# Kernel tuning notes

Measured on AMD Instinct MI355X. Metric: run time of the kernel, lower is better.

## Reference

```python
import jax, jax.numpy as jnp
import numpy as np

B, NX, NY, CIN = 4, 128, 128, 64
D, H = 64, 8  # out_channels, nhead
EPS = 1e-5


def setup_inputs() -> dict:
    key = jax.random.key(0)
    ks = jax.random.split(key, 12)
    s_in = 1.0 / np.sqrt(CIN)
    s_hd = 1.0 / np.sqrt(H * D)
    return {
        "v": jax.random.normal(ks[0], (B, NX, NY, CIN), jnp.float32),
        "Wq_w": jax.random.uniform(ks[1], (CIN, H * D), jnp.float32, -s_in, s_in),
        "Wq_b": jax.random.uniform(ks[2], (H * D,), jnp.float32, -s_in, s_in),
        "Wk_w": jax.random.uniform(ks[3], (CIN, H * D), jnp.float32, -s_in, s_in),
        "Wk_b": jax.random.uniform(ks[4], (H * D,), jnp.float32, -s_in, s_in),
        "Wv_w": jax.random.uniform(ks[5], (CIN, H * D), jnp.float32, -s_in, s_in),
        "Wv_b": jax.random.uniform(ks[6], (H * D,), jnp.float32, -s_in, s_in),
        "lnq_g": jnp.ones((H, D), jnp.float32),
        "lnq_b": jnp.zeros((H, D), jnp.float32),
        "lnk_g": jnp.ones((H, D), jnp.float32),
        "lnk_b": jnp.zeros((H, D), jnp.float32),
        "Wo_w": jax.random.uniform(ks[7], (H * D, D), jnp.float32, -s_hd, s_hd),
        "Wo_b": jax.random.uniform(ks[8], (D,), jnp.float32, -s_hd, s_hd),
    }


def _layernorm(x, gamma, beta):
    # x: [b,h,n,d]; gamma/beta: [h,d] (per-head params)
    mu = jnp.mean(x, axis=-1, keepdims=True)
    var = jnp.mean(jnp.square(x - mu), axis=-1, keepdims=True)
    xn = (x - mu) * jax.lax.rsqrt(var + EPS)
    return xn * gamma[None, :, None, :] + beta[None, :, None, :]


def reference(v, Wq_w, Wq_b, Wk_w, Wk_b, Wv_w, Wv_b,
              lnq_g, lnq_b, lnk_g, lnk_b, Wo_w, Wo_b):
    b, nx, ny, _ = v.shape
    n = nx * ny
    vf = v.reshape(b, n, -1)  # [b, n, cin]
    # QKV projections -> [b, h, n, d]
    def proj(w, bias):
        y = vf @ w + bias  # [b, n, h*d]
        return y.reshape(b, n, H, D).transpose(0, 2, 1, 3)
    Q = _layernorm(proj(Wq_w, Wq_b), lnq_g, lnq_b)
    K = _layernorm(proj(Wk_w, Wk_b), lnk_g, lnk_b)
    V = proj(Wv_w, Wv_b)
    # Non-softmax linear attention: (Q K^T) V == Q (K^T V); use O(n d^2) form
    kv = jnp.einsum('bhnd,bhne->bhde', K, V)      # [b,h,d,d]
    attn = jnp.einsum('bhmd,bhde->bhme', Q, kv)   # [b,h,n,d]
    attn = attn.transpose(0, 2, 1, 3).reshape(b, n, H * D)
    out = (attn @ Wo_w + Wo_b) / n
    return out.reshape(b, nx, ny, D)
```

## Files before the change

### kernel.cpp

```cpp
#include <hip/hip_runtime.h>

typedef __attribute__((ext_vector_type(8))) short bhalf8;
typedef __attribute__((ext_vector_type(4))) float f32x4;

#define MFMA_BF16 __builtin_amdgcn_mfma_f32_16x16x32_bf16

namespace {

constexpr int   NPIX  = 16384;
constexpr float EPSV  = 1e-5f;
constexpr float INV64 = 1.0f / 64.0f;
constexpr float INV_N = 1.0f / 16384.0f;

__device__ __forceinline__ unsigned short f2bf(float f) {
    unsigned int u = __builtin_bit_cast(unsigned int, f);
    u += 0x7fffu + ((u >> 16) & 1u);
    return (unsigned short)(u >> 16);
}

__global__ void k0_vsum(const float* __restrict__ v, float* __restrict__ vsum)
{
    const int slab = blockIdx.x, b = blockIdx.y, t = threadIdx.x;
    const int c = t & 63, po = t >> 6;
    const float* src = v + ((size_t)b * NPIX + slab * 256 + po * 64) * 64 + c;
    float s = 0.f;
#pragma unroll 8
    for (int i = 0; i < 64; ++i) s += src[(size_t)i * 64];
    __shared__ float red[4][64];
    red[po][c] = s;
    __syncthreads();
    if (t < 64) {
        float x = red[0][t] + red[1][t] + red[2][t] + red[3][t];
        atomicAdd(vsum + b * 64 + t, x);
    }
}

__global__ __launch_bounds__(256, 2)
void k1_kv(const float* __restrict__ v,  const float* __restrict__ Wk,
           const float* __restrict__ bk, const float* __restrict__ Wv,
           const float* __restrict__ bv, float* __restrict__ kvG)
{
    const int ch = blockIdx.x, h = blockIdx.y, b = blockIdx.z;
    const int t = threadIdx.x;
    const int w = t >> 6, l = t & 63, g = l >> 4, m16 = l & 15;

    __shared__ float kvred[4][4096];
    char* zone = reinterpret_cast<char*>(&kvred[0][0]) + w * 14848;
    unsigned short* vz  = reinterpret_cast<unsigned short*>(zone);
    unsigned short* ktz = reinterpret_cast<unsigned short*>(zone + 4608);
    unsigned short* vtz = reinterpret_cast<unsigned short*>(zone + 9728);

    bhalf8 wkf[4][2], wvf[4][2];
    const int wcol = h * 64 + m16;
#pragma unroll
    for (int mt = 0; mt < 4; ++mt)
#pragma unroll
      for (int ks = 0; ks < 2; ++ks)
#pragma unroll
        for (int j = 0; j < 8; ++j) {
            const int c = 32 * ks + 8 * g + j;
            wkf[mt][ks][j] = (short)f2bf(Wk[c * 512 + wcol + 16 * mt]);
            wvf[mt][ks][j] = (short)f2bf(Wv[c * 512 + wcol + 16 * mt]);
        }
    float bkr[4][4], bvr[4][4];
#pragma unroll
    for (int mt = 0; mt < 4; ++mt)
#pragma unroll
      for (int q = 0; q < 4; ++q) {
          const int d = 16 * mt + 4 * g + q;
          bkr[mt][q] = bk[h * 64 + d];
          bvr[mt][q] = bv[h * 64 + d];
      }

    f32x4 kv[4][4];
#pragma unroll
    for (int i = 0; i < 4; ++i)
#pragma unroll
      for (int j2 = 0; j2 < 4; ++j2) kv[i][j2] = f32x4{0.f, 0.f, 0.f, 0.f};

    const float* vbase = v + ((size_t)b * NPIX + ch * 1024 + w * 256) * 64;
    const int sp = l >> 1, sh = l & 1;

    for (int s = 0; s < 8; ++s) {
        {
            const float4* src = reinterpret_cast<const float4*>(
                vbase + (size_t)(s * 32 + sp) * 64 + sh * 32);
            unsigned short* dst = vz + sp * 72 + sh * 32;
#pragma unroll
            for (int qq = 0; qq < 8; ++qq) {
                float4 x = src[qq];
                ushort4 o;
                o.x = f2bf(x.x); o.y = f2bf(x.y); o.z = f2bf(x.z); o.w = f2bf(x.w);
                *reinterpret_cast<ushort4*>(dst + qq * 4) = o;
            }
        }
        __builtin_amdgcn_sched_barrier(0);
        bhalf8 vf[2][2];
#pragma unroll
        for (int nt = 0; nt < 2; ++nt)
#pragma unroll
          for (int ks = 0; ks < 2; ++ks)
            vf[nt][ks] = *reinterpret_cast<const bhalf8*>(
                vz + (16 * nt + m16) * 72 + 32 * ks + 8 * g);

#pragma unroll
        for (int mt = 0; mt < 4; ++mt)
#pragma unroll
          for (int nt = 0; nt < 2; ++nt) {
              f32x4 a = {0.f, 0.f, 0.f, 0.f};
              a = MFMA_BF16(wvf[mt][0], vf[nt][0], a, 0, 0, 0);
              a = MFMA_BF16(wvf[mt][1], vf[nt][1], a, 0, 0, 0);
#pragma unroll
              for (int q = 0; q < 4; ++q)
                  vtz[(16 * mt + 4 * g + q) * 40 + 16 * nt + m16] =
                      f2bf(a[q] + bvr[mt][q]);
          }

        f32x4 pa[4][2];
#pragma unroll
        for (int mt = 0; mt < 4; ++mt)
#pragma unroll
          for (int nt = 0; nt < 2; ++nt) {
              f32x4 a = {0.f, 0.f, 0.f, 0.f};
              a = MFMA_BF16(wkf[mt][0], vf[nt][0], a, 0, 0, 0);
              a = MFMA_BF16(wkf[mt][1], vf[nt][1], a, 0, 0, 0);
#pragma unroll
              for (int q = 0; q < 4; ++q) a[q] += bkr[mt][q];
              pa[mt][nt] = a;
          }
#pragma unroll
        for (int nt = 0; nt < 2; ++nt) {
            float s1 = 0.f, s2 = 0.f;
#pragma unroll
            for (int mt = 0; mt < 4; ++mt)
#pragma unroll
              for (int q = 0; q < 4; ++q) {
                  float x = pa[mt][nt][q]; s1 += x; s2 = fmaf(x, x, s2);
              }
            s1 += __shfl_xor(s1, 16, 64); s1 += __shfl_xor(s1, 32, 64);
            s2 += __shfl_xor(s2, 16, 64); s2 += __shfl_xor(s2, 32, 64);
            const float mu = s1 * INV64;
            const float rs = rsqrtf(fmaxf(s2 * INV64 - mu * mu, 0.f) + EPSV);
#pragma unroll
            for (int mt = 0; mt < 4; ++mt)
#pragma unroll
              for (int q = 0; q < 4; ++q)
                  ktz[(16 * mt + 4 * g + q) * 40 + 16 * nt + m16] =
                      f2bf((pa[mt][nt][q] - mu) * rs);
        }
        __builtin_amdgcn_sched_barrier(0);

        bhalf8 ka[4], vb2[4];
#pragma unroll
        for (int mt = 0; mt < 4; ++mt)
            ka[mt] = *reinterpret_cast<const bhalf8*>(ktz + (16 * mt + m16) * 40 + 8 * g);
#pragma unroll
        for (int nt = 0; nt < 4; ++nt)
            vb2[nt] = *reinterpret_cast<const bhalf8*>(vtz + (16 * nt + m16) * 40 + 8 * g);
#pragma unroll
        for (int mt = 0; mt < 4; ++mt)
#pragma unroll
          for (int nt = 0; nt < 4; ++nt)
              kv[mt][nt] = MFMA_BF16(ka[mt], vb2[nt], kv[mt][nt], 0, 0, 0);
        __builtin_amdgcn_sched_barrier(0);
    }

    __syncthreads();
#pragma unroll
    for (int mt = 0; mt < 4; ++mt)
#pragma unroll
      for (int nt = 0; nt < 4; ++nt)
#pragma unroll
        for (int q = 0; q < 4; ++q)
            kvred[w][(16 * mt + 4 * g + q) * 64 + 16 * nt + m16] = kv[mt][nt][q];
    __syncthreads();
    float* dstg = kvG + ((size_t)(b * 8 + h)) * 4096;
#pragma unroll
    for (int i = 0; i < 16; ++i) {
        const int idx = i * 256 + t;
        const float srd = kvred[0][idx] + kvred[1][idx] + kvred[2][idx] + kvred[3][idx];
        atomicAdd(dstg + idx, srd);
    }
}

__global__ void k2_mix(const float* __restrict__ kvG,  const float* __restrict__ vsum,
                       const float* __restrict__ Wv,   const float* __restrict__ bv,
                       const float* __restrict__ lnkg, const float* __restrict__ lnkb,
                       const float* __restrict__ lnqg, const float* __restrict__ lnqb,
                       const float* __restrict__ Wo,   const float* __restrict__ Wob,
                       unsigned short* __restrict__ MTp, float* __restrict__ cbeta)
{
    const int h = blockIdx.x, b = blockIdx.y, t = threadIdx.x;
    __shared__ float kvs[64][65], wos[64][65], mts[64][65], Svs[64], us[64];
    const int r = t >> 2, c0 = (t & 3) * 16;
    const float* kg = kvG + ((size_t)(b * 8 + h)) * 4096;
#pragma unroll
    for (int i = 0; i < 16; i += 4) {
        float4 x = *reinterpret_cast<const float4*>(kg + r * 64 + c0 + i);
        kvs[r][c0+i] = x.x; kvs[r][c0+i+1] = x.y; kvs[r][c0+i+2] = x.z; kvs[r][c0+i+3] = x.w;
    }
#pragma unroll
    for (int i = 0; i < 16; i += 4) {
        float4 x = *reinterpret_cast<const float4*>(Wo + ((size_t)(h * 64) + r) * 64 + c0 + i);
        wos[r][c0+i] = x.x; wos[r][c0+i+1] = x.y; wos[r][c0+i+2] = x.z; wos[r][c0+i+3] = x.w;
    }
    if (t < 64) {
        float s = 16384.f * bv[h * 64 + t];
        for (int cc = 0; cc < 64; ++cc)
            s = fmaf(vsum[b * 64 + cc], Wv[cc * 512 + h * 64 + t], s);
        Svs[t] = s;
    }
    __syncthreads();
    {
        const float gk = lnkg[h * 64 + r], bk2 = lnkb[h * 64 + r];
#pragma unroll
        for (int i = 0; i < 16; ++i)
            kvs[r][c0 + i] = gk * kvs[r][c0 + i] + bk2 * Svs[c0 + i];
    }
    __syncthreads();
    if (t < 64) {
        float s = 0.f;
        for (int dd = 0; dd < 64; ++dd) s = fmaf(lnqb[h * 64 + dd], kvs[dd][t], s);
        us[t] = s;
    }
    float mrow[16];
#pragma unroll
    for (int i = 0; i < 16; ++i) mrow[i] = 0.f;
    for (int e2 = 0; e2 < 64; ++e2) {
        const float kr = kvs[r][e2];
#pragma unroll
        for (int i = 0; i < 16; ++i) mrow[i] = fmaf(kr, wos[e2][c0 + i], mrow[i]);
    }
    {
        const float gq = lnqg[h * 64 + r] * INV_N;
#pragma unroll
        for (int i = 0; i < 16; ++i) mts[c0 + i][r] = gq * mrow[i];
    }
    __syncthreads();
    if (t < 64) {
        float s = 0.f;
        for (int e2 = 0; e2 < 64; ++e2) s = fmaf(us[e2], wos[e2][t], s);
        atomicAdd(cbeta + b * 64 + t, s * INV_N);
        if (h == 0) atomicAdd(cbeta + b * 64 + t, Wob[t] * INV_N);
    }
    unsigned short* mo = MTp + ((size_t)(b * 8 + h)) * 4096 + r * 64 + c0;
#pragma unroll
    for (int i = 0; i < 16; i += 4) {
        ushort4 o;
        o.x = f2bf(mts[r][c0+i]);   o.y = f2bf(mts[r][c0+i+1]);
        o.z = f2bf(mts[r][c0+i+2]); o.w = f2bf(mts[r][c0+i+3]);
        *reinterpret_cast<ushort4*>(mo + i) = o;
    }
}

__global__ __launch_bounds__(256, 2)
void k3_out(const float* __restrict__ v,  const float* __restrict__ Wq,
            const float* __restrict__ bq, const unsigned short* __restrict__ MTp,
            const float* __restrict__ cbeta, float* __restrict__ out)
{
    const int blk = blockIdx.x, b = blockIdx.y;
    const int t = threadIdx.x, w = t >> 6, l = t & 63, g = l >> 4, m16 = l & 15;

    __shared__ unsigned short smem[4][4608];
    unsigned short* vz  = smem[w];
    unsigned short* qtz = smem[w] + 2304;

    const int px0 = blk * 128 + w * 32;
    const float* vbase = v + ((size_t)b * NPIX + px0) * 64;
    const int sp = l >> 1, sh = l & 1;
    {
        const float4* src = reinterpret_cast<const float4*>(vbase + (size_t)sp * 64 + sh * 32);
        unsigned short* dst = vz + sp * 72 + sh * 32;
#pragma unroll
        for (int qq = 0; qq < 8; ++qq) {
            float4 x = src[qq];
            ushort4 o;
            o.x = f2bf(x.x); o.y = f2bf(x.y); o.z = f2bf(x.z); o.w = f2bf(x.w);
            *reinterpret_cast<ushort4*>(dst + qq * 4) = o;
        }
    }
    __builtin_amdgcn_sched_barrier(0);
    bhalf8 vf[2][2];
#pragma unroll
    for (int nt = 0; nt < 2; ++nt)
#pragma unroll
      for (int ks = 0; ks < 2; ++ks)
        vf[nt][ks] = *reinterpret_cast<const bhalf8*>(
            vz + (16 * nt + m16) * 72 + 32 * ks + 8 * g);

    f32x4 outa[4][2];
#pragma unroll
    for (int i = 0; i < 4; ++i)
#pragma unroll
      for (int j2 = 0; j2 < 2; ++j2) outa[i][j2] = f32x4{0.f, 0.f, 0.f, 0.f};

    for (int h = 0; h < 8; ++h) {
        bhalf8 wqf[4][2];
        float bqr[4][4];
        const int wcol = h * 64 + m16;
#pragma unroll
        for (int mt = 0; mt < 4; ++mt)
#pragma unroll
          for (int ks = 0; ks < 2; ++ks)
#pragma unroll
            for (int j = 0; j < 8; ++j) {
                const int c = 32 * ks + 8 * g + j;
                wqf[mt][ks][j] = (short)f2bf(Wq[c * 512 + wcol + 16 * mt]);
            }
#pragma unroll
        for (int mt = 0; mt < 4; ++mt)
#pragma unroll
          for (int q = 0; q < 4; ++q) bqr[mt][q] = bq[h * 64 + 16 * mt + 4 * g + q];

        bhalf8 mf[4][2];
        const unsigned short* mtb = MTp + ((size_t)(b * 8 + h)) * 4096;
#pragma unroll
        for (int mt = 0; mt < 4; ++mt)
#pragma unroll
          for (int ks = 0; ks < 2; ++ks)
            mf[mt][ks] = *reinterpret_cast<const bhalf8*>(
                mtb + (16 * mt + m16) * 64 + 32 * ks + 8 * g);

        f32x4 qa[4][2];
#pragma unroll
        for (int mt = 0; mt < 4; ++mt)
#pragma unroll
          for (int nt = 0; nt < 2; ++nt) {
              f32x4 a = {0.f, 0.f, 0.f, 0.f};
              a = MFMA_BF16(wqf[mt][0], vf[nt][0], a, 0, 0, 0);
              a = MFMA_BF16(wqf[mt][1], vf[nt][1], a, 0, 0, 0);
#pragma unroll
              for (int q = 0; q < 4; ++q) a[q] += bqr[mt][q];
              qa[mt][nt] = a;
          }
#pragma unroll
        for (int nt = 0; nt < 2; ++nt) {
            float s1 = 0.f, s2 = 0.f;
#pragma unroll
            for (int mt = 0; mt < 4; ++mt)
#pragma unroll
              for (int q = 0; q < 4; ++q) {
                  float x = qa[mt][nt][q]; s1 += x; s2 = fmaf(x, x, s2);
              }
            s1 += __shfl_xor(s1, 16, 64); s1 += __shfl_xor(s1, 32, 64);
            s2 += __shfl_xor(s2, 16, 64); s2 += __shfl_xor(s2, 32, 64);
            const float mu = s1 * INV64;
            const float rs = rsqrtf(fmaxf(s2 * INV64 - mu * mu, 0.f) + EPSV);
#pragma unroll
            for (int mt = 0; mt < 4; ++mt)
#pragma unroll
              for (int q = 0; q < 4; ++q)
                  qtz[(16 * nt + m16) * 72 + 16 * mt + 4 * g + q] =
                      f2bf((qa[mt][nt][q] - mu) * rs);
        }
        __builtin_amdgcn_sched_barrier(0);
        bhalf8 qb[2][2];
#pragma unroll
        for (int nt = 0; nt < 2; ++nt)
#pragma unroll
          for (int ks = 0; ks < 2; ++ks)
            qb[nt][ks] = *reinterpret_cast<const bhalf8*>(
                qtz + (16 * nt + m16) * 72 + 32 * ks + 8 * g);
#pragma unroll
        for (int mt = 0; mt < 4; ++mt)
#pragma unroll
          for (int nt = 0; nt < 2; ++nt) {
              outa[mt][nt] = MFMA_BF16(mf[mt][0], qb[nt][0], outa[mt][nt], 0, 0, 0);
              outa[mt][nt] = MFMA_BF16(mf[mt][1], qb[nt][1], outa[mt][nt], 0, 0, 0);
          }
        __builtin_amdgcn_sched_barrier(0);
    }

    float* ob = out + ((size_t)b * NPIX + px0) * 64;
#pragma unroll
    for (int mt = 0; mt < 4; ++mt)
#pragma unroll
      for (int q = 0; q < 4; ++q) {
          const int e = 16 * mt + 4 * g + q;
          const float add = cbeta[b * 64 + e];
#pragma unroll
          for (int nt = 0; nt < 2; ++nt)
              ob[(size_t)(16 * nt + m16) * 64 + e] = outa[mt][nt][q] + add;
      }
}

}

extern "C" void kernel_launch(void* const* d_in, const int* in_sizes, int n_in,
                              void* d_out, int out_size, void* d_ws, size_t ws_size,
                              hipStream_t stream)
{
    const float* v     = (const float*)d_in[0];
    const float* Wq_w  = (const float*)d_in[1];
    const float* Wq_b  = (const float*)d_in[2];
    const float* Wk_w  = (const float*)d_in[3];
    const float* Wk_b  = (const float*)d_in[4];
    const float* Wv_w  = (const float*)d_in[5];
    const float* Wv_b  = (const float*)d_in[6];
    const float* lnq_g = (const float*)d_in[7];
    const float* lnq_b = (const float*)d_in[8];
    const float* lnk_g = (const float*)d_in[9];
    const float* lnk_b = (const float*)d_in[10];
    const float* Wo_w  = (const float*)d_in[11];
    const float* Wo_b  = (const float*)d_in[12];
    float* out = (float*)d_out;

    float* kvG   = (float*)d_ws;
    float* vsum  = kvG + 131072;
    float* cbeta = vsum + 256;
    unsigned short* MTp = (unsigned short*)(cbeta + 256);

    hipMemsetAsync(d_ws, 0, (131072 + 512) * sizeof(float), stream);
    k0_vsum<<<dim3(64, 4), 256, 0, stream>>>(v, vsum);
    k1_kv<<<dim3(16, 8, 4), 256, 0, stream>>>(v, Wk_w, Wk_b, Wv_w, Wv_b, kvG);
    k2_mix<<<dim3(8, 4), 256, 0, stream>>>(kvG, vsum, Wv_w, Wv_b, lnk_g, lnk_b,
                                           lnq_g, lnq_b, Wo_w, Wo_b, MTp, cbeta);
    k3_out<<<dim3(128, 4), 256, 0, stream>>>(v, Wq_w, Wq_b, MTp, cbeta, out);
}
```

Before: 187.4 us.

## Prepack bf16 weights, drop LDS staging, and split K-layernorm mean into correction term

```diff
diff --git a/kernel.cpp b/kernel.cpp
--- a/kernel.cpp
+++ b/kernel.cpp
@@ -1,4 +1,5 @@
 #include <hip/hip_runtime.h>
+#include <hip/hip_bf16.h>
 
 typedef __attribute__((ext_vector_type(8))) short bhalf8;
 typedef __attribute__((ext_vector_type(4))) float f32x4;
@@ -12,196 +13,300 @@
 constexpr float INV64 = 1.0f / 64.0f;
 constexpr float INV_N = 1.0f / 16384.0f;
 
-__device__ __forceinline__ unsigned short f2bf(float f) {
+constexpr int KV1_OFF   = 0;
+constexpr int T_OFF     = 131072;
+constexpr int VSUM_OFF  = 131072 + 2048;
+constexpr int CBETA_OFF = 131072 + 2048 + 256;
+constexpr int FZERO_CNT = 131072 + 2048 + 256 + 256;
+
+__device__ __host__ __forceinline__ unsigned short f2bf(float f) {
     unsigned int u = __builtin_bit_cast(unsigned int, f);
     u += 0x7fffu + ((u >> 16) & 1u);
     return (unsigned short)(u >> 16);
 }
 
+union B8 { bhalf8 v; unsigned int u[4]; ushort4 s4[2]; };
+
+__device__ __forceinline__ unsigned int pk2(float a, float b) {
+    union { __hip_bfloat162 h; unsigned int u; } x;
+    x.h = __float22bfloat162_rn(float2{a, b});
+    return x.u;
+}
+
 __global__ void k0_vsum(const float* __restrict__ v, float* __restrict__ vsum)
 {
-    const int slab = blockIdx.x, b = blockIdx.y, t = threadIdx.x;
-    const int c = t & 63, po = t >> 6;
-    const float* src = v + ((size_t)b * NPIX + slab * 256 + po * 64) * 64 + c;
-    float s = 0.f;
-#pragma unroll 8
-    for (int i = 0; i < 64; ++i) s += src[(size_t)i * 64];
-    __shared__ float red[4][64];
-    red[po][c] = s;
+    const int blk = blockIdx.x, b = blockIdx.y, t = threadIdx.x;
+    const int c4 = t & 15, p = t >> 4;
+    float4 a = make_float4(0.f, 0.f, 0.f, 0.f);
+    const float* base = v + ((size_t)b * NPIX + blk * 128) * 64 + c4 * 4;
+#pragma unroll
+    for (int i = 0; i < 8; ++i) {
+        const float4 x = *reinterpret_cast<const float4*>(base + (size_t)(p * 8 + i) * 64);
+        a.x += x.x; a.y += x.y; a.z += x.z; a.w += x.w;
+    }
+    __shared__ float4 red[16][16];
+    red[p][c4] = a;
     __syncthreads();
-    if (t < 64) {
-        float x = red[0][t] + red[1][t] + red[2][t] + red[3][t];
-        atomicAdd(vsum + b * 64 + t, x);
+    if (t < 16) {
+        float4 s = red[0][t];
+#pragma unroll
+        for (int i = 1; i < 16; ++i) {
+            const float4 x = red[i][t];
+            s.x += x.x; s.y += x.y; s.z += x.z; s.w += x.w;
+        }
+        atomicAdd(vsum + b * 64 + t * 4 + 0, s.x);
+        atomicAdd(vsum + b * 64 + t * 4 + 1, s.y);
+        atomicAdd(vsum + b * 64 + t * 4 + 2, s.z);
+        atomicAdd(vsum + b * 64 + t * 4 + 3, s.w);
+    }
+}
+
+__global__ void kpack(const float* __restrict__ Wk, const float* __restrict__ Wv,
+                      const float* __restrict__ Wq,
+                      unsigned short* __restrict__ wkpk, unsigned short* __restrict__ wvpk,
+                      unsigned short* __restrict__ wqpk, unsigned short* __restrict__ wksumb)
+{
+    const int w = blockIdx.x >> 3, h = blockIdx.x & 7, t = threadIdx.x;
+    const float* W = (w == 0) ? Wk : (w == 1) ? Wv : Wq;
+    unsigned short* dst = (w == 0) ? wkpk : (w == 1) ? wvpk : wqpk;
+
+#pragma unroll
+    for (int i = 0; i < 2; ++i) {
+        const int f = t * 2 + i;
+        const int nt = (f >> 7) & 3, ks = (f >> 6) & 1, l = f & 63;
+        const int g = l >> 4, m = l & 15;
+        ushort4 o0, o1;
+        unsigned short tmp[8];
+#pragma unroll
+        for (int j = 0; j < 8; ++j)
+            tmp[j] = f2bf(W[(size_t)(32 * ks + 8 * g + j) * 512 + h * 64 + 16 * nt + m]);
+        o0 = make_ushort4(tmp[0], tmp[1], tmp[2], tmp[3]);
+        o1 = make_ushort4(tmp[4], tmp[5], tmp[6], tmp[7]);
+        unsigned short* d = dst + ((size_t)((h * 4 + nt) * 2 + ks)) * 512 + l * 8;
+        *reinterpret_cast<ushort4*>(d)     = o0;
+        *reinterpret_cast<ushort4*>(d + 4) = o1;
+    }
+    if (w == 0 && t < 64) {
+        float s = 0.f;
+        const float* row = Wk + (size_t)t * 512 + h * 64;
+#pragma unroll
+        for (int d = 0; d < 64; ++d) s += row[d];
+        wksumb[h * 64 + t] = f2bf(s);
     }
 }
 
 __global__ __launch_bounds__(256, 2)
-void k1_kv(const float* __restrict__ v,  const float* __restrict__ Wk,
-           const float* __restrict__ bk, const float* __restrict__ Wv,
-           const float* __restrict__ bv, float* __restrict__ kvG)
+void k1_kv(const float* __restrict__ v,
+           const unsigned short* __restrict__ wkpk, const unsigned short* __restrict__ wvpk,
+           const unsigned short* __restrict__ wksumb,
+           const float* __restrict__ bk, const float* __restrict__ bv,
+           float* __restrict__ kv1, float* __restrict__ tG)
 {
     const int ch = blockIdx.x, h = blockIdx.y, b = blockIdx.z;
-    const int t = threadIdx.x;
-    const int w = t >> 6, l = t & 63, g = l >> 4, m16 = l & 15;
+    const int t = threadIdx.x, w = t >> 6, l = t & 63, g = l >> 4, m16 = l & 15;
+
+    bhalf8 wkB[4][2], wvB[4][2], wks[2];
+#pragma unroll
+    for (int nt = 0; nt < 4; ++nt)
+#pragma unroll
+      for (int ks = 0; ks < 2; ++ks) {
+          wkB[nt][ks] = *reinterpret_cast<const bhalf8*>(
+              wkpk + ((size_t)((h * 4 + nt) * 2 + ks)) * 512 + l * 8);
+          wvB[nt][ks] = *reinterpret_cast<const bhalf8*>(
+              wvpk + ((size_t)((h * 4 + nt) * 2 + ks)) * 512 + l * 8);
+      }
+#pragma unroll
+    for (int ks = 0; ks < 2; ++ks)
+        wks[ks] = *reinterpret_cast<const bhalf8*>(wksumb + h * 64 + 32 * ks + 8 * g);
+
+    float bksum;
+    {
+        float bl = bk[h * 64 + l];
+#pragma unroll
+        for (int m = 1; m < 64; m <<= 1) bl += __shfl_xor(bl, m, 64);
+        bksum = bl;
+    }
+    float bkv[4], bvv[4];
+#pragma unroll
+    for (int nt = 0; nt < 4; ++nt) {
+        bkv[nt] = bk[h * 64 + 16 * nt + m16];
+        bvv[nt] = bv[h * 64 + 16 * nt + m16];
+    }
+
+    f32x4 kv[4][4];
+#pragma unroll
+    for (int i = 0; i < 4; ++i)
+#pragma unroll
+      for (int j = 0; j < 4; ++j) kv[i][j] = f32x4{0.f, 0.f, 0.f, 0.f};
+    float tl[4] = {0.f, 0.f, 0.f, 0.f};
+
+    const float* vw = v + ((size_t)b * NPIX + ch * 1024 + w * 256) * 64;
+
+    for (int s = 0; s < 8; ++s) {
+        B8 vA[2][2];
+#pragma unroll
+        for (int mt = 0; mt < 2; ++mt)
+#pragma unroll
+          for (int ks = 0; ks < 2; ++ks) {
+              const float* src = vw + (size_t)(s * 32 + 16 * mt + m16) * 64 + 32 * ks + 8 * g;
+              const float4 a = *reinterpret_cast<const float4*>(src);
+              const float4 c = *reinterpret_cast<const float4*>(src + 4);
+              vA[mt][ks].u[0] = pk2(a.x, a.y); vA[mt][ks].u[1] = pk2(a.z, a.w);
+              vA[mt][ks].u[2] = pk2(c.x, c.y); vA[mt][ks].u[3] = pk2(c.z, c.w);
+          }
+
+        f32x4 kq[2][4];
+#pragma unroll
+        for (int mt = 0; mt < 2; ++mt)
+#pragma unroll
+          for (int nt = 0; nt < 4; ++nt) {
+              f32x4 a = {0.f, 0.f, 0.f, 0.f};
+              a = MFMA_BF16(vA[mt][0].v, wkB[nt][0], a, 0, 0, 0);
+              a = MFMA_BF16(vA[mt][1].v, wkB[nt][1], a, 0, 0, 0);
+#pragma unroll
+              for (int q = 0; q < 4; ++q) a[q] += bkv[nt];
+              kq[mt][nt] = a;
+          }
+        f32x4 st[2];
+#pragma unroll
+        for (int mt = 0; mt < 2; ++mt) {
+            f32x4 a = {0.f, 0.f, 0.f, 0.f};
+            a = MFMA_BF16(vA[mt][0].v, wks[0], a, 0, 0, 0);
+            a = MFMA_BF16(vA[mt][1].v, wks[1], a, 0, 0, 0);
+            st[mt] = a;
+        }
+        f32x4 s2p[2];
+#pragma unroll
+        for (int mt = 0; mt < 2; ++mt) {
+#pragma unroll
+            for (int q = 0; q < 4; ++q) {
+                float acc = kq[mt][0][q] * kq[mt][0][q];
+                acc = fmaf(kq[mt][1][q], kq[mt][1][q], acc);
+                acc = fmaf(kq[mt][2][q], kq[mt][2][q], acc);
+                acc = fmaf(kq[mt][3][q], kq[mt][3][q], acc);
+                s2p[mt][q] = acc;
+            }
+        }
+#pragma unroll
+        for (int mt = 0; mt < 2; ++mt)
+#pragma unroll
+          for (int q = 0; q < 4; ++q) {
+              float x = s2p[mt][q];
+              x += __shfl_xor(x, 1, 64);
+              x += __shfl_xor(x, 2, 64);
+              x += __shfl_xor(x, 4, 64);
+              x += __shfl_xor(x, 8, 64);
+              s2p[mt][q] = x;
+          }
+        f32x4 rsv[2], cmu[2];
+#pragma unroll
+        for (int mt = 0; mt < 2; ++mt)
+#pragma unroll
+          for (int q = 0; q < 4; ++q) {
+              const float mu  = (st[mt][q] + bksum) * INV64;
+              const float var = s2p[mt][q] * INV64 - mu * mu;
+              const float rs  = rsqrtf(fmaxf(var, 0.f) + EPSV);
+              rsv[mt][q] = rs;
+              cmu[mt][q] = mu * rs;
+          }
+        B8 ka[4];
+#pragma unroll
+        for (int MT = 0; MT < 4; ++MT) {
+            ka[MT].u[0] = pk2(kq[0][MT][0] * rsv[0][0], kq[0][MT][1] * rsv[0][1]);
+            ka[MT].u[1] = pk2(kq[0][MT][2] * rsv[0][2], kq[0][MT][3] * rsv[0][3]);
+            ka[MT].u[2] = pk2(kq[1][MT][0] * rsv[1][0], kq[1][MT][1] * rsv[1][1]);
+            ka[MT].u[3] = pk2(kq[1][MT][2] * rsv[1][2], kq[1][MT][3] * rsv[1][3]);
+        }
+        f32x4 vq[2][4];
+#pragma unroll
+        for (int mt = 0; mt < 2; ++mt)
+#pragma unroll
+          for (int nt = 0; nt < 4; ++nt) {
+              f32x4 a = {0.f, 0.f, 0.f, 0.f};
+              a = MFMA_BF16(vA[mt][0].v, wvB[nt][0], a, 0, 0, 0);
+              a = MFMA_BF16(vA[mt][1].v, wvB[nt][1], a, 0, 0, 0);
+#pragma unroll
+              for (int q = 0; q < 4; ++q) a[q] += bvv[nt];
+              vq[mt][nt] = a;
+          }
+#pragma unroll
+        for (int nt = 0; nt < 4; ++nt) {
+            float acc = tl[nt];
+#pragma unroll
+            for (int mt = 0; mt < 2; ++mt)
+#pragma unroll
+              for (int q = 0; q < 4; ++q)
+                  acc = fmaf(cmu[mt][q], vq[mt][nt][q], acc);
+            tl[nt] = acc;
+        }
+        B8 vb[4];
+#pragma unroll
+        for (int NT = 0; NT < 4; ++NT) {
+            vb[NT].u[0] = pk2(vq[0][NT][0], vq[0][NT][1]);
+            vb[NT].u[1] = pk2(vq[0][NT][2], vq[0][NT][3]);
+            vb[NT].u[2] = pk2(vq[1][NT][0], vq[1][NT][1]);
+            vb[NT].u[3] = pk2(vq[1][NT][2], vq[1][NT][3]);
+        }
+#pragma unroll
+        for (int MT = 0; MT < 4; ++MT)
+#pragma unroll
+          for (int NT = 0; NT < 4; ++NT)
+              kv[MT][NT] = MFMA_BF16(ka[MT].v, vb[NT].v, kv[MT][NT], 0, 0, 0);
+    }
+
+#pragma unroll
+    for (int nt = 0; nt < 4; ++nt) {
+        float x = tl[nt];
+        x += __shfl_xor(x, 16, 64);
+        x += __shfl_xor(x, 32, 64);
+        tl[nt] = x;
+    }
+    if (g == 0) {
+        float* td = tG + ((size_t)(b * 8 + h)) * 64;
+#pragma unroll
+        for (int nt = 0; nt < 4; ++nt) atomicAdd(td + 16 * nt + m16, tl[nt]);
+    }
 
     __shared__ float kvred[4][4096];
-    char* zone = reinterpret_cast<char*>(&kvred[0][0]) + w * 14848;
-    unsigned short* vz  = reinterpret_cast<unsigned short*>(zone);
-    unsigned short* ktz = reinterpret_cast<unsigned short*>(zone + 4608);
-    unsigned short* vtz = reinterpret_cast<unsigned short*>(zone + 9728);
-
-    bhalf8 wkf[4][2], wvf[4][2];
-    const int wcol = h * 64 + m16;
-#pragma unroll
-    for (int mt = 0; mt < 4; ++mt)
-#pragma unroll
-      for (int ks = 0; ks < 2; ++ks)
-#pragma unroll
-        for (int j = 0; j < 8; ++j) {
-            const int c = 32 * ks + 8 * g + j;
-            wkf[mt][ks][j] = (short)f2bf(Wk[c * 512 + wcol + 16 * mt]);
-            wvf[mt][ks][j] = (short)f2bf(Wv[c * 512 + wcol + 16 * mt]);
-        }
-    float bkr[4][4], bvr[4][4];
-#pragma unroll
-    for (int mt = 0; mt < 4; ++mt)
-#pragma unroll
-      for (int q = 0; q < 4; ++q) {
-          const int d = 16 * mt + 4 * g + q;
-          bkr[mt][q] = bk[h * 64 + d];
-          bvr[mt][q] = bv[h * 64 + d];
-      }
-
-    f32x4 kv[4][4];
-#pragma unroll
-    for (int i = 0; i < 4; ++i)
-#pragma unroll
-      for (int j2 = 0; j2 < 4; ++j2) kv[i][j2] = f32x4{0.f, 0.f, 0.f, 0.f};
-
-    const float* vbase = v + ((size_t)b * NPIX + ch * 1024 + w * 256) * 64;
-    const int sp = l >> 1, sh = l & 1;
-
-    for (int s = 0; s < 8; ++s) {
-        {
-            const float4* src = reinterpret_cast<const float4*>(
-                vbase + (size_t)(s * 32 + sp) * 64 + sh * 32);
-            unsigned short* dst = vz + sp * 72 + sh * 32;
-#pragma unroll
-            for (int qq = 0; qq < 8; ++qq) {
-                float4 x = src[qq];
-                ushort4 o;
-                o.x = f2bf(x.x); o.y = f2bf(x.y); o.z = f2bf(x.z); o.w = f2bf(x.w);
-                *reinterpret_cast<ushort4*>(dst + qq * 4) = o;
-            }
-        }
-        __builtin_amdgcn_sched_barrier(0);
-        bhalf8 vf[2][2];
-#pragma unroll
-        for (int nt = 0; nt < 2; ++nt)
-#pragma unroll
-          for (int ks = 0; ks < 2; ++ks)
-            vf[nt][ks] = *reinterpret_cast<const bhalf8*>(
-                vz + (16 * nt + m16) * 72 + 32 * ks + 8 * g);
-
-#pragma unroll
-        for (int mt = 0; mt < 4; ++mt)
-#pragma unroll
-          for (int nt = 0; nt < 2; ++nt) {
-              f32x4 a = {0.f, 0.f, 0.f, 0.f};
-              a = MFMA_BF16(wvf[mt][0], vf[nt][0], a, 0, 0, 0);
-              a = MFMA_BF16(wvf[mt][1], vf[nt][1], a, 0, 0, 0);
-#pragma unroll
-              for (int q = 0; q < 4; ++q)
-                  vtz[(16 * mt + 4 * g + q) * 40 + 16 * nt + m16] =
-                      f2bf(a[q] + bvr[mt][q]);
-          }
-
-        f32x4 pa[4][2];
-#pragma unroll
-        for (int mt = 0; mt < 4; ++mt)
-#pragma unroll
-          for (int nt = 0; nt < 2; ++nt) {
-              f32x4 a = {0.f, 0.f, 0.f, 0.f};
-              a = MFMA_BF16(wkf[mt][0], vf[nt][0], a, 0, 0, 0);
-              a = MFMA_BF16(wkf[mt][1], vf[nt][1], a, 0, 0, 0);
-#pragma unroll
-              for (int q = 0; q < 4; ++q) a[q] += bkr[mt][q];
-              pa[mt][nt] = a;
-          }
-#pragma unroll
-        for (int nt = 0; nt < 2; ++nt) {
-            float s1 = 0.f, s2 = 0.f;
-#pragma unroll
-            for (int mt = 0; mt < 4; ++mt)
-#pragma unroll
-              for (int q = 0; q < 4; ++q) {
-                  float x = pa[mt][nt][q]; s1 += x; s2 = fmaf(x, x, s2);
-              }
-            s1 += __shfl_xor(s1, 16, 64); s1 += __shfl_xor(s1, 32, 64);
-            s2 += __shfl_xor(s2, 16, 64); s2 += __shfl_xor(s2, 32, 64);
-            const float mu = s1 * INV64;
-            const float rs = rsqrtf(fmaxf(s2 * INV64 - mu * mu, 0.f) + EPSV);
-#pragma unroll
-            for (int mt = 0; mt < 4; ++mt)
-#pragma unroll
-              for (int q = 0; q < 4; ++q)
-                  ktz[(16 * mt + 4 * g + q) * 40 + 16 * nt + m16] =
-                      f2bf((pa[mt][nt][q] - mu) * rs);
-        }
-        __builtin_amdgcn_sched_barrier(0);
-
-        bhalf8 ka[4], vb2[4];
-#pragma unroll
-        for (int mt = 0; mt < 4; ++mt)
-            ka[mt] = *reinterpret_cast<const bhalf8*>(ktz + (16 * mt + m16) * 40 + 8 * g);
-#pragma unroll
-        for (int nt = 0; nt < 4; ++nt)
-            vb2[nt] = *reinterpret_cast<const bhalf8*>(vtz + (16 * nt + m16) * 40 + 8 * g);
-#pragma unroll
-        for (int mt = 0; mt < 4; ++mt)
-#pragma unroll
-          for (int nt = 0; nt < 4; ++nt)
-              kv[mt][nt] = MFMA_BF16(ka[mt], vb2[nt], kv[mt][nt], 0, 0, 0);
-        __builtin_amdgcn_sched_barrier(0);
-    }
-
     __syncthreads();
 #pragma unroll
-    for (int mt = 0; mt < 4; ++mt)
-#pragma unroll
-      for (int nt = 0; nt < 4; ++nt)
+    for (int MT = 0; MT < 4; ++MT)
+#pragma unroll
+      for (int NT = 0; NT < 4; ++NT)
 #pragma unroll
         for (int q = 0; q < 4; ++q)
-            kvred[w][(16 * mt + 4 * g + q) * 64 + 16 * nt + m16] = kv[mt][nt][q];
+            kvred[w][(16 * MT + 4 * g + q) * 64 + 16 * NT + m16] = kv[MT][NT][q];
     __syncthreads();
-    float* dstg = kvG + ((size_t)(b * 8 + h)) * 4096;
+    float* dstg = kv1 + ((size_t)(b * 8 + h)) * 4096;
 #pragma unroll
     for (int i = 0; i < 16; ++i) {
         const int idx = i * 256 + t;
-        const float srd = kvred[0][idx] + kvred[1][idx] + kvred[2][idx] + kvred[3][idx];
-        atomicAdd(dstg + idx, srd);
-    }
-}
-
-__global__ void k2_mix(const float* __restrict__ kvG,  const float* __restrict__ vsum,
+        atomicAdd(dstg + idx,
+                  kvred[0][idx] + kvred[1][idx] + kvred[2][idx] + kvred[3][idx]);
+    }
+}
+
+__global__ void k2_mix(const float* __restrict__ kv1,  const float* __restrict__ tG,
+                       const float* __restrict__ vsum,
                        const float* __restrict__ Wv,   const float* __restrict__ bv,
                        const float* __restrict__ lnkg, const float* __restrict__ lnkb,
                        const float* __restrict__ lnqg, const float* __restrict__ lnqb,
                        const float* __restrict__ Wo,   const float* __restrict__ Wob,
-                       unsigned short* __restrict__ MTp, float* __restrict__ cbeta)
+                       unsigned short* __restrict__ mpk, float* __restrict__ cbeta)
 {
     const int h = blockIdx.x, b = blockIdx.y, t = threadIdx.x;
-    __shared__ float kvs[64][65], wos[64][65], mts[64][65], Svs[64], us[64];
+    __shared__ float kvs[64][65], wos[64][65], mls[64][65], Svs[64], us[64];
     const int r = t >> 2, c0 = (t & 3) * 16;
-    const float* kg = kvG + ((size_t)(b * 8 + h)) * 4096;
+    const float* kg = kv1 + ((size_t)(b * 8 + h)) * 4096;
+    const float* td = tG + ((size_t)(b * 8 + h)) * 64;
 #pragma unroll
     for (int i = 0; i < 16; i += 4) {
-        float4 x = *reinterpret_cast<const float4*>(kg + r * 64 + c0 + i);
+        const float4 x = *reinterpret_cast<const float4*>(kg + r * 64 + c0 + i);
         kvs[r][c0+i] = x.x; kvs[r][c0+i+1] = x.y; kvs[r][c0+i+2] = x.z; kvs[r][c0+i+3] = x.w;
     }
 #pragma unroll
     for (int i = 0; i < 16; i += 4) {
-        float4 x = *reinterpret_cast<const float4*>(Wo + ((size_t)(h * 64) + r) * 64 + c0 + i);
+        const float4 x = *reinterpret_cast<const float4*>(Wo + ((size_t)(h * 64) + r) * 64 + c0 + i);
         wos[r][c0+i] = x.x; wos[r][c0+i+1] = x.y; wos[r][c0+i+2] = x.z; wos[r][c0+i+3] = x.w;
     }
     if (t < 64) {
@@ -214,8 +319,10 @@
     {
         const float gk = lnkg[h * 64 + r], bk2 = lnkb[h * 64 + r];
 #pragma unroll
-        for (int i = 0; i < 16; ++i)
-            kvs[r][c0 + i] = gk * kvs[r][c0 + i] + bk2 * Svs[c0 + i];
+        for (int i = 0; i < 16; ++i) {
+            const int e = c0 + i;
+            kvs[r][e] = gk * (kvs[r][e] - td[e]) + bk2 * Svs[e];
+        }
     }
     __syncthreads();
     if (t < 64) {
@@ -234,7 +341,7 @@
     {
         const float gq = lnqg[h * 64 + r] * INV_N;
 #pragma unroll
-        for (int i = 0; i < 16; ++i) mts[c0 + i][r] = gq * mrow[i];
+        for (int i = 0; i < 16; ++i) mls[r][c0 + i] = gq * mrow[i];
     }
     __syncthreads();
     if (t < 64) {
@@ -243,83 +350,72 @@
         atomicAdd(cbeta + b * 64 + t, s * INV_N);
         if (h == 0) atomicAdd(cbeta + b * 64 + t, Wob[t] * INV_N);
     }
-    unsigned short* mo = MTp + ((size_t)(b * 8 + h)) * 4096 + r * 64 + c0;
-#pragma unroll
-    for (int i = 0; i < 16; i += 4) {
-        ushort4 o;
-        o.x = f2bf(mts[r][c0+i]);   o.y = f2bf(mts[r][c0+i+1]);
-        o.z = f2bf(mts[r][c0+i+2]); o.w = f2bf(mts[r][c0+i+3]);
-        *reinterpret_cast<ushort4*>(mo + i) = o;
+#pragma unroll
+    for (int i = 0; i < 2; ++i) {
+        const int f = t * 2 + i;
+        const int nt = (f >> 7) & 3, ks = (f >> 6) & 1, l = f & 63;
+        const int g = l >> 4, m = l & 15;
+        unsigned short o[8];
+#pragma unroll
+        for (int j = 0; j < 8; ++j) {
+            const int d = 32 * ks + 16 * (j >> 2) + 4 * g + (j & 3);
+            o[j] = f2bf(mls[d][16 * nt + m]);
+        }
+        unsigned short* dd = mpk + ((size_t)((b * 8 + h) * 8 + nt * 2 + ks)) * 512 + l * 8;
+        *reinterpret_cast<ushort4*>(dd)     = make_ushort4(o[0], o[1], o[2], o[3]);
+        *reinterpret_cast<ushort4*>(dd + 4) = make_ushort4(o[4], o[5], o[6], o[7]);
     }
 }
 
 __global__ __launch_bounds__(256, 2)
-void k3_out(const float* __restrict__ v,  const float* __restrict__ Wq,
-            const float* __restrict__ bq, const unsigned short* __restrict__ MTp,
-            const float* __restrict__ cbeta, float* __restrict__ out)
+void k3_out(const float* __restrict__ v,
+            const unsigned short* __restrict__ wqpk, const float* __restrict__ bq,
+            const unsigned short* __restrict__ mpk,  const float* __restrict__ cbeta,
+            float* __restrict__ out)
 {
     const int blk = blockIdx.x, b = blockIdx.y;
     const int t = threadIdx.x, w = t >> 6, l = t & 63, g = l >> 4, m16 = l & 15;
-
-    __shared__ unsigned short smem[4][4608];
-    unsigned short* vz  = smem[w];
-    unsigned short* qtz = smem[w] + 2304;
-
-    const int px0 = blk * 128 + w * 32;
-    const float* vbase = v + ((size_t)b * NPIX + px0) * 64;
-    const int sp = l >> 1, sh = l & 1;
-    {
-        const float4* src = reinterpret_cast<const float4*>(vbase + (size_t)sp * 64 + sh * 32);
-        unsigned short* dst = vz + sp * 72 + sh * 32;
-#pragma unroll
-        for (int qq = 0; qq < 8; ++qq) {
-            float4 x = src[qq];
-            ushort4 o;
-            o.x = f2bf(x.x); o.y = f2bf(x.y); o.z = f2bf(x.z); o.w = f2bf(x.w);
-            *reinterpret_cast<ushort4*>(dst + qq * 4) = o;
-        }
-    }
-    __builtin_amdgcn_sched_barrier(0);
-    bhalf8 vf[2][2];
+    const size_t px0 = (size_t)b * NPIX + blk * 128 + w * 32;
+
+    B8 vB[2][2];
 #pragma unroll
     for (int nt = 0; nt < 2; ++nt)
 #pragma unroll
-      for (int ks = 0; ks < 2; ++ks)
-        vf[nt][ks] = *reinterpret_cast<const bhalf8*>(
-            vz + (16 * nt + m16) * 72 + 32 * ks + 8 * g);
-
-    f32x4 outa[4][2];
-#pragma unroll
-    for (int i = 0; i < 4; ++i)
-#pragma unroll
-      for (int j2 = 0; j2 < 2; ++j2) outa[i][j2] = f32x4{0.f, 0.f, 0.f, 0.f};
+      for (int ks = 0; ks < 2; ++ks) {
+          const float* src = v + (px0 + 16 * nt + m16) * 64 + 32 * ks + 8 * g;
+          const float4 a = *reinterpret_cast<const float4*>(src);
+          const float4 c = *reinterpret_cast<const float4*>(src + 4);
+          vB[nt][ks].u[0] = pk2(a.x, a.y); vB[nt][ks].u[1] = pk2(a.z, a.w);
+          vB[nt][ks].u[2] = pk2(c.x, c.y); vB[nt][ks].u[3] = pk2(c.z, c.w);
+      }
+    float cbv[4];
+#pragma unroll
+    for (int nt = 0; nt < 4; ++nt) cbv[nt] = cbeta[b * 64 + 16 * nt + m16];
+
+    f32x4 outa[2][4];
+#pragma unroll
+    for (int i = 0; i < 2; ++i)
+#pragma unroll
+      for (int j = 0; j < 4; ++j) outa[i][j] = f32x4{0.f, 0.f, 0.f, 0.f};
 
     for (int h = 0; h < 8; ++h) {
-        bhalf8 wqf[4][2];
-        float bqr[4][4];
-        const int wcol = h * 64 + m16;
+        bhalf8 wqA[4][2], mB[2][4];
 #pragma unroll
         for (int mt = 0; mt < 4; ++mt)
 #pragma unroll
           for (int ks = 0; ks < 2; ++ks)
-#pragma unroll
-            for (int j = 0; j < 8; ++j) {
-                const int c = 32 * ks + 8 * g + j;
-                wqf[mt][ks][j] = (short)f2bf(Wq[c * 512 + wcol + 16 * mt]);
-            }
+            wqA[mt][ks] = *reinterpret_cast<const bhalf8*>(
+                wqpk + ((size_t)((h * 4 + mt) * 2 + ks)) * 512 + l * 8);
+#pragma unroll
+        for (int ks = 0; ks < 2; ++ks)
+#pragma unroll
+          for (int nt = 0; nt < 4; ++nt)
+            mB[ks][nt] = *reinterpret_cast<const bhalf8*>(
+                mpk + ((size_t)((b * 8 + h) * 8 + nt * 2 + ks)) * 512 + l * 8);
+        float4 bq4[4];
 #pragma unroll
         for (int mt = 0; mt < 4; ++mt)
-#pragma unroll
-          for (int q = 0; q < 4; ++q) bqr[mt][q] = bq[h * 64 + 16 * mt + 4 * g + q];
-
-        bhalf8 mf[4][2];
-        const unsigned short* mtb = MTp + ((size_t)(b * 8 + h)) * 4096;
-#pragma unroll
-        for (int mt = 0; mt < 4; ++mt)
-#pragma unroll
-          for (int ks = 0; ks < 2; ++ks)
-            mf[mt][ks] = *reinterpret_cast<const bhalf8*>(
-                mtb + (16 * mt + m16) * 64 + 32 * ks + 8 * g);
+            bq4[mt] = *reinterpret_cast<const float4*>(bq + h * 64 + 16 * mt + 4 * g);
 
         f32x4 qa[4][2];
 #pragma unroll
@@ -327,12 +423,13 @@
 #pragma unroll
           for (int nt = 0; nt < 2; ++nt) {
               f32x4 a = {0.f, 0.f, 0.f, 0.f};
-              a = MFMA_BF16(wqf[mt][0], vf[nt][0], a, 0, 0, 0);
-              a = MFMA_BF16(wqf[mt][1], vf[nt][1], a, 0, 0, 0);
-#pragma unroll
-              for (int q = 0; q < 4; ++q) a[q] += bqr[mt][q];
+              a = MFMA_BF16(wqA[mt][0], vB[nt][0].v, a, 0, 0, 0);
+              a = MFMA_BF16(wqA[mt][1], vB[nt][1].v, a, 0, 0, 0);
+              a[0] += bq4[mt].x; a[1] += bq4[mt].y;
+              a[2] += bq4[mt].z; a[3] += bq4[mt].w;
               qa[mt][nt] = a;
           }
+        float mu[2], rs[2];
 #pragma unroll
         for (int nt = 0; nt < 2; ++nt) {
             float s1 = 0.f, s2 = 0.f;
@@ -340,47 +437,45 @@
             for (int mt = 0; mt < 4; ++mt)
 #pragma unroll
               for (int q = 0; q < 4; ++q) {
-                  float x = qa[mt][nt][q]; s1 += x; s2 = fmaf(x, x, s2);
+                  const float x = qa[mt][nt][q];
+                  s1 += x; s2 = fmaf(x, x, s2);
               }
             s1 += __shfl_xor(s1, 16, 64); s1 += __shfl_xor(s1, 32, 64);
             s2 += __shfl_xor(s2, 16, 64); s2 += __shfl_xor(s2, 32, 64);
-            const float mu = s1 * INV64;
-            const float rs = rsqrtf(fmaxf(s2 * INV64 - mu * mu, 0.f) + EPSV);
-#pragma unroll
-            for (int mt = 0; mt < 4; ++mt)
-#pragma unroll
-              for (int q = 0; q < 4; ++q)
-                  qtz[(16 * nt + m16) * 72 + 16 * mt + 4 * g + q] =
-                      f2bf((qa[mt][nt][q] - mu) * rs);
-        }
-        __builtin_amdgcn_sched_barrier(0);
-        bhalf8 qb[2][2];
-#pragma unroll
-        for (int nt = 0; nt < 2; ++nt)
-#pragma unroll
-          for (int ks = 0; ks < 2; ++ks)
-            qb[nt][ks] = *reinterpret_cast<const bhalf8*>(
-                qtz + (16 * nt + m16) * 72 + 32 * ks + 8 * g);
-#pragma unroll
-        for (int mt = 0; mt < 4; ++mt)
-#pragma unroll
-          for (int nt = 0; nt < 2; ++nt) {
-              outa[mt][nt] = MFMA_BF16(mf[mt][0], qb[nt][0], outa[mt][nt], 0, 0, 0);
-              outa[mt][nt] = MFMA_BF16(mf[mt][1], qb[nt][1], outa[mt][nt], 0, 0, 0);
-          }
-        __builtin_amdgcn_sched_barrier(0);
-    }
-
-    float* ob = out + ((size_t)b * NPIX + px0) * 64;
-#pragma unroll
-    for (int mt = 0; mt < 4; ++mt)
+            mu[nt] = s1 * INV64;
+            rs[nt] = rsqrtf(fmaxf(s2 * INV64 - mu[nt] * mu[nt], 0.f) + EPSV);
+        }
+        B8 ka[2][2];
+#pragma unroll
+        for (int MT = 0; MT < 2; ++MT)
+#pragma unroll
+          for (int ks = 0; ks < 2; ++ks) {
+              ka[MT][ks].u[0] = pk2((qa[2*ks+0][MT][0] - mu[MT]) * rs[MT],
+                                    (qa[2*ks+0][MT][1] - mu[MT]) * rs[MT]);
+              ka[MT][ks].u[1] = pk2((qa[2*ks+0][MT][2] - mu[MT]) * rs[MT],
+                                    (qa[2*ks+0][MT][3] - mu[MT]) * rs[MT]);
+              ka[MT][ks].u[2] = pk2((qa[2*ks+1][MT][0] - mu[MT]) * rs[MT],
+                                    (qa[2*ks+1][MT][1] - mu[MT]) * rs[MT]);
+              ka[MT][ks].u[3] = pk2((qa[2*ks+1][MT][2] - mu[MT]) * rs[MT],
+                                    (qa[2*ks+1][MT][3] - mu[MT]) * rs[MT]);
+          }
+#pragma unroll
+        for (int MT = 0; MT < 2; ++MT)
+#pragma unroll
+          for (int nt = 0; nt < 4; ++nt) {
+              outa[MT][nt] = MFMA_BF16(ka[MT][0].v, mB[0][nt], outa[MT][nt], 0, 0, 0);
+              outa[MT][nt] = MFMA_BF16(ka[MT][1].v, mB[1][nt], outa[MT][nt], 0, 0, 0);
+          }
+    }
+
+#pragma unroll
+    for (int MT = 0; MT < 2; ++MT)
 #pragma unroll
       for (int q = 0; q < 4; ++q) {
-          const int e = 16 * mt + 4 * g + q;
-          const float add = cbeta[b * 64 + e];
-#pragma unroll
-          for (int nt = 0; nt < 2; ++nt)
-              ob[(size_t)(16 * nt + m16) * 64 + e] = outa[mt][nt][q] + add;
+          float* orow = out + (px0 + 16 * MT + 4 * g + q) * 64;
+#pragma unroll
+          for (int nt = 0; nt < 4; ++nt)
+              orow[16 * nt + m16] = outa[MT][nt][q] + cbv[nt];
       }
 }
 
@@ -405,15 +500,25 @@
     const float* Wo_b  = (const float*)d_in[12];
     float* out = (float*)d_out;
 
-    float* kvG   = (float*)d_ws;
-    float* vsum  = kvG + 131072;
-    float* cbeta = vsum + 256;
-    unsigned short* MTp = (unsigned short*)(cbeta + 256);
-
-    hipMemsetAsync(d_ws, 0, (131072 + 512) * sizeof(float), stream);
-    k0_vsum<<<dim3(64, 4), 256, 0, stream>>>(v, vsum);
-    k1_kv<<<dim3(16, 8, 4), 256, 0, stream>>>(v, Wk_w, Wk_b, Wv_w, Wv_b, kvG);
-    k2_mix<<<dim3(8, 4), 256, 0, stream>>>(kvG, vsum, Wv_w, Wv_b, lnk_g, lnk_b,
-                                           lnq_g, lnq_b, Wo_w, Wo_b, MTp, cbeta);
-    k3_out<<<dim3(128, 4), 256, 0, stream>>>(v, Wq_w, Wq_b, MTp, cbeta, out);
-}
+    float* wsf   = (float*)d_ws;
+    float* kv1   = wsf + KV1_OFF;
+    float* tG    = wsf + T_OFF;
+    float* vsum  = wsf + VSUM_OFF;
+    float* cbeta = wsf + CBETA_OFF;
+    unsigned short* base_s = (unsigned short*)(wsf + FZERO_CNT);
+    unsigned short* wkpk   = base_s;
+    unsigned short* wvpk   = base_s + 32768;
+    unsigned short* wqpk   = base_s + 65536;
+    unsigned short* wksumb = base_s + 98304;
+    unsigned short* mpk    = base_s + 98816;
+
+    hipMemsetAsync(d_ws, 0, (size_t)FZERO_CNT * sizeof(float), stream);
+    k0_vsum<<<dim3(128, 4), 256, 0, stream>>>(v, vsum);
+    kpack<<<24, 256, 0, stream>>>(Wk_w, Wv_w, Wq_w, wkpk, wvpk, wqpk, wksumb);
+    k1_kv<<<dim3(16, 8, 4), 256, 0, stream>>>(v, wkpk, wvpk, wksumb, Wk_b, Wv_b,
+                                              kv1, tG);
+    k2_mix<<<dim3(8, 4), 256, 0, stream>>>(kv1, tG, vsum, Wv_w, Wv_b,
+                                           lnk_g, lnk_b, lnq_g, lnq_b,
+                                           Wo_w, Wo_b, mpk, cbeta);
+    k3_out<<<dim3(128, 4), 256, 0, stream>>>(v, wqpk, Wq_b, mpk, cbeta, out);
+}
```

Result: faster. 178.9 us (-4.5%).
